# Performance work log

Hardware: AMD Instinct MI355X
Metric: run time of the kernel (lower is better)

Reference implementation:

```python
import jax, jax.numpy as jnp
import numpy as np

# CSSA config (index=0): H=W=64, strip windows h_spa=64, w_spa=8, heads=4, C=64
B, HW, C, HEADS = 32, 64, 64, 4
HS, WS = 64, 8          # h_spa, w_spa
HD = C // HEADS          # head_dim = 16
WIN = HS * WS            # 512 tokens per window
SCALE = HD ** -0.5


def setup_inputs() -> dict:
    key = jax.random.key(0)
    k1, k2, k3 = jax.random.split(key, 3)
    qkv = jax.random.normal(k1, (3, B, HW * HW, C), dtype=jnp.float32)
    w_conv = jax.random.normal(k2, (C, 1, 3, 3), dtype=jnp.float32) * 0.1
    b_conv = jax.random.normal(k3, (C,), dtype=jnp.float32) * 0.1
    return {"qkv": qkv, "w_conv": w_conv, "b_conv": b_conv}


def _to_img(x):
    # [B, N, C] -> [B, C, H, W]
    return jnp.transpose(x.reshape(B, HW, HW, C), (0, 3, 1, 2))


def _img2window_heads(x):
    img = _to_img(x)
    img = img.reshape(B, C, HW // HS, HS, HW // WS, WS)
    win = jnp.transpose(img, (0, 2, 4, 3, 5, 1)).reshape(-1, WIN, C)
    return jnp.transpose(win.reshape(-1, WIN, HEADS, HD), (0, 2, 1, 3))


def _v_windows(x):
    # [B, N, C] -> [B*nWin, C, h_spa, w_spa] (image-layout windows for conv)
    img = _to_img(x)
    img = img.reshape(B, C, HW // HS, HS, HW // WS, WS)
    return jnp.transpose(img, (0, 2, 4, 1, 3, 5)).reshape(-1, C, HS, WS)


def reference(qkv, w_conv, b_conv):
    q, k, v = qkv[0], qkv[1], qkv[2]
    qh = _img2window_heads(q) * SCALE
    kh = _img2window_heads(k)
    vw = _v_windows(v)                           # [Bw, C, HS, WS]
    # depthwise 3x3 conv LePE
    lepe = jax.lax.conv_general_dilated(
        vw, w_conv, window_strides=(1, 1), padding=((1, 1), (1, 1)),
        feature_group_count=C,
        dimension_numbers=("NCHW", "OIHW", "NCHW")) + b_conv[None, :, None, None]
    Bw = vw.shape[0]
    lepe = jnp.transpose(lepe.reshape(Bw, HEADS, HD, WIN), (0, 1, 3, 2))
    vh = jnp.transpose(vw.reshape(Bw, HEADS, HD, WIN), (0, 1, 3, 2))
    attn = jax.nn.softmax(jnp.einsum("whqd,whkd->whqk", qh, kh), axis=-1)
    x = jnp.einsum("whqk,whkd->whqd", attn, vh) + lepe
    x = jnp.transpose(x, (0, 2, 1, 3)).reshape(Bw, WIN, C)
    # window2spa
    x = x.reshape(B, HW // HS, HW // WS, HS, WS, C)
    x = jnp.transpose(x, (0, 1, 3, 2, 4, 5)).reshape(B, HW * HW, C)
    return x
```

## Files before the change

kernel.cpp:

```cpp
#include <hip/hip_runtime.h>
#include <stdint.h>

#define NB    32
#define CCH   64
#define HD    16
#define WIN   512
#define KSTR  72
#define VSTR  520
#define PSTR  40

typedef __attribute__((ext_vector_type(8))) short          short8;
typedef __attribute__((ext_vector_type(4))) float          f32x4;
typedef __attribute__((ext_vector_type(4))) unsigned short us4;

__device__ __forceinline__ float bf2f(unsigned short u) {
    union { unsigned int i; float f; } x; x.i = ((unsigned int)u) << 16; return x.f;
}
__device__ __forceinline__ unsigned short f2bf(float f) {
    union { float f; unsigned int i; } x; x.f = f;
    unsigned int r = x.i + 0x7FFFu + ((x.i >> 16) & 1u);
    return (unsigned short)(r >> 16);
}

__global__ __launch_bounds__(512, 2)
void CSSA_69355131896243_kernel(const float* __restrict__ qkv,
                                const float* __restrict__ wconv,
                                const float* __restrict__ bconv,
                                float* __restrict__ out)
{
    __shared__ unsigned short Kl[WIN * KSTR];
    __shared__ unsigned short Vt[CCH * VSTR];
    __shared__ unsigned short Pl[8 * 16 * PSTR];

    const int tid  = threadIdx.x;
    const int wave = tid >> 6;
    const int lane = tid & 63;
    const int quad = lane >> 4;
    const int l15  = lane & 15;

    const int win = blockIdx.x;
    const int b   = win >> 3;
    const int wx  = win & 7;

    const size_t ONE  = (size_t)NB * 4096 * CCH;
    const size_t base = ((size_t)b * 4096 + (size_t)wx * 8) * CCH;

    {
        const float* gK = qkv + ONE     + base;
        const float* gV = qkv + 2 * ONE + base;
        const int tokb = lane >> 4;
        const int c0   = (lane & 15) * 4;
        for (int r = 0; r < 8; ++r) {
            const int y = r * 8 + wave;
            #pragma unroll
            for (int half = 0; half < 2; ++half) {
                const int t = y * 8 + half * 4 + tokb;
                const size_t goff = (size_t)y * 4096 + half * 256 + lane * 4;
                f32x4 kd = *(const f32x4*)(gK + goff);
                f32x4 vd = *(const f32x4*)(gV + goff);
                us4 kb;
                #pragma unroll
                for (int j = 0; j < 4; ++j) kb[j] = f2bf(kd[j]);
                *(us4*)(&Kl[t * KSTR + c0]) = kb;
                #pragma unroll
                for (int j = 0; j < 4; ++j) Vt[(c0 + j) * VSTR + t] = f2bf(vd[j]);
            }
        }
    }
    __syncthreads();

    const int h  = wave >> 1;
    const int qh = wave & 1;
    const int ch = h * HD + l15;

    float wr[9];
    #pragma unroll
    for (int i = 0; i < 9; ++i) wr[i] = wconv[ch * 9 + i];
    const float bias = bconv[ch];

    unsigned short* Pw = &Pl[wave * 16 * PSTR];
    const float* gQ = qkv + base;
    const float EC = 0.25f * 1.44269504088896341f;

    for (int pass = 0; pass < 2; ++pass) {
        const int q0 = qh * 256 + pass * 128;

        short8 qf[8];
        #pragma unroll
        for (int t = 0; t < 8; ++t) {
            if (quad < 2) {
                const int q = q0 + t * 16 + l15;
                const float* p = gQ + ((size_t)(q >> 3) * 64 + (q & 7)) * CCH + h * HD + quad * 8;
                f32x4 a = *(const f32x4*)p;
                f32x4 c = *(const f32x4*)(p + 4);
                short8 f;
                #pragma unroll
                for (int j = 0; j < 4; ++j) {
                    f[j]     = (short)f2bf(a[j]);
                    f[j + 4] = (short)f2bf(c[j]);
                }
                qf[t] = f;
            } else {
                qf[t] = (short8)0;
            }
        }

        f32x4 acc[8];
        f32x4 lp[8];
        #pragma unroll
        for (int t = 0; t < 8; ++t) { acc[t] = (f32x4)0.0f; lp[t] = (f32x4)0.0f; }

        for (int c = 0; c < 16; ++c) {
            const int k0 = c * 32;
            short8 kf0 = (short8)0, kf1 = (short8)0;
            if (quad < 2) {
                kf0 = *(const short8*)(&Kl[(k0 + l15)      * KSTR + h * HD + quad * 8]);
                kf1 = *(const short8*)(&Kl[(k0 + 16 + l15) * KSTR + h * HD + quad * 8]);
            }
            const short8 vf = *(const short8*)(&Vt[ch * VSTR + k0 + quad * 8]);

            #pragma unroll
            for (int t = 0; t < 8; ++t) {
                f32x4 s0 = __builtin_amdgcn_mfma_f32_16x16x32_bf16(qf[t], kf0, (f32x4)0.0f, 0, 0, 0);
                f32x4 s1 = __builtin_amdgcn_mfma_f32_16x16x32_bf16(qf[t], kf1, (f32x4)0.0f, 0, 0, 0);
                float p0[4], p1[4];
                #pragma unroll
                for (int j = 0; j < 4; ++j) {
                    p0[j] = __builtin_amdgcn_exp2f(s0[j] * EC);
                    p1[j] = __builtin_amdgcn_exp2f(s1[j] * EC);
                    lp[t][j] += p0[j] + p1[j];
                }
                #pragma unroll
                for (int j = 0; j < 4; ++j) {
                    Pw[(quad * 4 + j) * PSTR + l15]      = f2bf(p0[j]);
                    Pw[(quad * 4 + j) * PSTR + 16 + l15] = f2bf(p1[j]);
                }
                const short8 pf = *(const short8*)(&Pw[l15 * PSTR + quad * 8]);
                acc[t] = __builtin_amdgcn_mfma_f32_16x16x32_bf16(pf, vf, acc[t], 0, 0, 0);
            }
        }

        #pragma unroll
        for (int t = 0; t < 8; ++t) {
            f32x4 l4 = lp[t];
            #pragma unroll
            for (int j = 0; j < 4; ++j) {
                float v = l4[j];
                v += __shfl_xor(v, 1, 64);
                v += __shfl_xor(v, 2, 64);
                v += __shfl_xor(v, 4, 64);
                v += __shfl_xor(v, 8, 64);
                l4[j] = __builtin_amdgcn_rcpf(v);
            }
            #pragma unroll
            for (int j = 0; j < 4; ++j) {
                const int q  = q0 + t * 16 + quad * 4 + j;
                const int y  = q >> 3;
                const int xp = q & 7;
                float lep = bias;
                #pragma unroll
                for (int dy = 0; dy < 3; ++dy) {
                    #pragma unroll
                    for (int dx = 0; dx < 3; ++dx) {
                        const int yy = y + dy - 1, xx = xp + dx - 1;
                        const bool ok = ((unsigned)yy < 64u) && ((unsigned)xx < 8u);
                        const int tt = (q + (dy - 1) * 8 + (dx - 1)) & 511;
                        const float vv = bf2f(Vt[ch * VSTR + tt]);
                        lep += (ok ? wr[dy * 3 + dx] : 0.0f) * vv;
                    }
                }
                const float o = acc[t][j] * l4[j] + lep;
                const size_t off = ((size_t)y * 64 + xp) * CCH + ch;
                out[base + off] = o;
            }
        }
    }
}

extern "C" void kernel_launch(void* const* d_in, const int* in_sizes, int n_in,
                              void* d_out, int out_size, void* d_ws, size_t ws_size,
                              hipStream_t stream) {
    const float* qkv   = (const float*)d_in[0];
    const float* wconv = (const float*)d_in[1];
    const float* bconv = (const float*)d_in[2];
    float* outp = (float*)d_out;
    hipLaunchKernelGGL(CSSA_69355131896243_kernel, dim3(256), dim3(512), 0, stream,
                       qkv, wconv, bconv, outp);
}
```

Before: 226.2 us.

## Split attention per head per block and use K=16 bf16 MFMA with transposed scores

Launches one block per (window, head) instead of one per window, which gives 1024 blocks of 256 threads and much smaller LDS per block. Scores are computed transposed (K times Q) with the 16x16x16 bf16 MFMA, so the probability tile feeds the PV MFMA straight from registers, removing the LDS round-trip for P. It also prescales Q, rounds to bf16 with a cheaper packed conversion, prefetches K/V fragments, stages conv weights in LDS, and writes outputs as float4 vectors. The trade-off is that each head block reloads its slice of K and V, rounding changes slightly, and the block order is remapped across the grid.

```diff
diff --git a/kernel.cpp b/kernel.cpp
--- a/kernel.cpp
+++ b/kernel.cpp
@@ -1,179 +1,226 @@
 #include <hip/hip_runtime.h>
 #include <stdint.h>
 
-#define NB    32
-#define CCH   64
-#define HD    16
-#define WIN   512
-#define KSTR  72
+#define KSTR2 20
 #define VSTR  520
-#define PSTR  40
-
-typedef __attribute__((ext_vector_type(8))) short          short8;
+
+typedef __attribute__((ext_vector_type(4))) short          short4v;
+typedef __attribute__((ext_vector_type(8))) short          short8v;
 typedef __attribute__((ext_vector_type(4))) float          f32x4;
 typedef __attribute__((ext_vector_type(4))) unsigned short us4;
 
+#define HAVE_MFMA16 __has_builtin(__builtin_amdgcn_mfma_f32_16x16x16bf16_1k)
+
 __device__ __forceinline__ float bf2f(unsigned short u) {
     union { unsigned int i; float f; } x; x.i = ((unsigned int)u) << 16; return x.f;
 }
 __device__ __forceinline__ unsigned short f2bf(float f) {
-    union { float f; unsigned int i; } x; x.f = f;
-    unsigned int r = x.i + 0x7FFFu + ((x.i >> 16) & 1u);
-    return (unsigned short)(r >> 16);
-}
-
-__global__ __launch_bounds__(512, 2)
+    union { float f; unsigned int u; } x; x.f = f;
+    return (unsigned short)((x.u + 0x8000u) >> 16);
+}
+__device__ __forceinline__ unsigned int pk2bf(float lo, float hi) {
+    union { float f; unsigned int u; } a, b; a.f = lo; b.f = hi;
+    return __builtin_amdgcn_perm(b.u + 0x8000u, a.u + 0x8000u, 0x07060302u);
+}
+
+__global__ __launch_bounds__(256, 4)
 void CSSA_69355131896243_kernel(const float* __restrict__ qkv,
                                 const float* __restrict__ wconv,
                                 const float* __restrict__ bconv,
                                 float* __restrict__ out)
 {
-    __shared__ unsigned short Kl[WIN * KSTR];
-    __shared__ unsigned short Vt[CCH * VSTR];
-    __shared__ unsigned short Pl[8 * 16 * PSTR];
+    __shared__ unsigned short Kl[512 * KSTR2];
+    __shared__ unsigned short Vt[16 * VSTR];
+    __shared__ float Wl[144];
+    __shared__ float Bl[16];
 
     const int tid  = threadIdx.x;
-    const int wave = tid >> 6;
-    const int lane = tid & 63;
-    const int quad = lane >> 4;
-    const int l15  = lane & 15;
-
-    const int win = blockIdx.x;
-    const int b   = win >> 3;
-    const int wx  = win & 7;
-
-    const size_t ONE  = (size_t)NB * 4096 * CCH;
-    const size_t base = ((size_t)b * 4096 + (size_t)wx * 8) * CCH;
+    const int wave = tid >> 6, lane = tid & 63, quad = lane >> 4, l15 = lane & 15;
+
+    const int bid = blockIdx.x;
+    const int win = (bid & 7) * 32 + ((bid >> 3) >> 2);
+    const int h   = (bid >> 3) & 3;
+    const int b   = win >> 3, wx = win & 7;
+
+    const size_t ONE  = (size_t)32 * 4096 * 64;
+    const size_t base = ((size_t)b * 4096 + (size_t)wx * 8) * 64;
+    const float* gQ = qkv + base;
+    const float* gK = qkv + ONE + base;
+    const float* gV = qkv + 2 * ONE + base;
+
+    if (tid < 144) Wl[tid] = wconv[h * 144 + tid];
+    if (tid < 16)  Bl[tid] = bconv[h * 16 + tid];
 
     {
-        const float* gK = qkv + ONE     + base;
-        const float* gV = qkv + 2 * ONE + base;
-        const int tokb = lane >> 4;
-        const int c0   = (lane & 15) * 4;
+        const int t4 = tid >> 2;
+        const int c4 = tid & 3;
         for (int r = 0; r < 8; ++r) {
-            const int y = r * 8 + wave;
-            #pragma unroll
-            for (int half = 0; half < 2; ++half) {
-                const int t = y * 8 + half * 4 + tokb;
-                const size_t goff = (size_t)y * 4096 + half * 256 + lane * 4;
-                f32x4 kd = *(const f32x4*)(gK + goff);
-                f32x4 vd = *(const f32x4*)(gV + goff);
-                us4 kb;
+            const int t = r * 64 + t4;
+            const size_t goff = (size_t)(t >> 3) * 4096 + (size_t)(t & 7) * 64 + h * 16 + c4 * 4;
+            f32x4 kd = *(const f32x4*)(gK + goff);
+            f32x4 vd = *(const f32x4*)(gV + goff);
+            us4 kb;
+            #pragma unroll
+            for (int j = 0; j < 4; ++j) kb[j] = f2bf(kd[j]);
+            *(us4*)(&Kl[t * KSTR2 + c4 * 4]) = kb;
+            #pragma unroll
+            for (int j = 0; j < 4; ++j) Vt[(c4 * 4 + j) * VSTR + t] = f2bf(vd[j]);
+        }
+    }
+
+    const float SCL = 0.25f * 1.44269504088896341f;
+#if HAVE_MFMA16
+    f32x4 qv[8];
+    #pragma unroll
+    for (int t = 0; t < 8; ++t) {
+        const int q = wave * 128 + t * 16 + l15;
+        qv[t] = *(const f32x4*)(gQ + (size_t)(q >> 3) * 4096 + (size_t)(q & 7) * 64 + h * 16 + quad * 4);
+    }
+#else
+    f32x4 qv0[8], qv1[8];
+    #pragma unroll
+    for (int t = 0; t < 8; ++t) {
+        const int q = wave * 128 + t * 16 + l15;
+        const size_t off = (size_t)(q >> 3) * 4096 + (size_t)(q & 7) * 64 + h * 16 + (quad & 1) * 8;
+        qv0[t] = *(const f32x4*)(gQ + off);
+        qv1[t] = *(const f32x4*)(gQ + off + 4);
+    }
+#endif
+    __syncthreads();
+
+#if HAVE_MFMA16
+    short4v qf[8];
+    #pragma unroll
+    for (int t = 0; t < 8; ++t) {
+        union { short4v s; unsigned int u[2]; } p;
+        p.u[0] = pk2bf(qv[t][0] * SCL, qv[t][1] * SCL);
+        p.u[1] = pk2bf(qv[t][2] * SCL, qv[t][3] * SCL);
+        qf[t] = p.s;
+    }
+#else
+    short8v qf[8];
+    #pragma unroll
+    for (int t = 0; t < 8; ++t) {
+        short8v f = (short8v)0;
+        if (quad < 2) {
+            union { short4v s; unsigned int u[2]; } pa, pb;
+            pa.u[0] = pk2bf(qv0[t][0] * SCL, qv0[t][1] * SCL);
+            pa.u[1] = pk2bf(qv0[t][2] * SCL, qv0[t][3] * SCL);
+            pb.u[0] = pk2bf(qv1[t][0] * SCL, qv1[t][1] * SCL);
+            pb.u[1] = pk2bf(qv1[t][2] * SCL, qv1[t][3] * SCL);
+            #pragma unroll
+            for (int i = 0; i < 4; ++i) { f[i] = pa.s[i]; f[4 + i] = pb.s[i]; }
+        }
+        qf[t] = f;
+    }
+#endif
+
+    f32x4 acc[8];
+    float lp[8];
+    #pragma unroll
+    for (int t = 0; t < 8; ++t) { acc[t] = (f32x4)0.0f; lp[t] = 0.0f; }
+
+#if HAVE_MFMA16
+    short4v kf = *(const short4v*)(&Kl[l15 * KSTR2 + quad * 4]);
+    short4v vf = *(const short4v*)(&Vt[l15 * VSTR + quad * 4]);
+    for (int c = 0; c < 32; ++c) {
+        const int kn = ((c + 1) & 31) * 16;
+        short4v kf_n = *(const short4v*)(&Kl[(kn + l15) * KSTR2 + quad * 4]);
+        short4v vf_n = *(const short4v*)(&Vt[l15 * VSTR + kn + quad * 4]);
+        #pragma unroll
+        for (int t = 0; t < 8; ++t) {
+            f32x4 s = __builtin_amdgcn_mfma_f32_16x16x16bf16_1k(kf, qf[t], (f32x4)0.0f, 0, 0, 0);
+            float p0 = __builtin_amdgcn_exp2f(s[0]);
+            float p1 = __builtin_amdgcn_exp2f(s[1]);
+            float p2 = __builtin_amdgcn_exp2f(s[2]);
+            float p3 = __builtin_amdgcn_exp2f(s[3]);
+            lp[t] += (p0 + p1) + (p2 + p3);
+            union { short4v s4; unsigned int u[2]; } pf;
+            pf.u[0] = pk2bf(p0, p1);
+            pf.u[1] = pk2bf(p2, p3);
+            acc[t] = __builtin_amdgcn_mfma_f32_16x16x16bf16_1k(vf, pf.s4, acc[t], 0, 0, 0);
+        }
+        kf = kf_n; vf = vf_n;
+    }
+#else
+    const int bidx0 = (((quad & 1) * 2) * 16 + l15) * 4;
+    const int bidx1 = bidx0 + 64;
+    for (int c = 0; c < 16; ++c) {
+        const int k0 = c * 32;
+        short8v kfA = (short8v)0, kfB = (short8v)0;
+        if (quad < 2) {
+            const short4v a0 = *(const short4v*)(&Kl[(k0 + l15) * KSTR2 + quad * 8]);
+            const short4v a1 = *(const short4v*)(&Kl[(k0 + l15) * KSTR2 + quad * 8 + 4]);
+            const short4v b0 = *(const short4v*)(&Kl[(k0 + 16 + l15) * KSTR2 + quad * 8]);
+            const short4v b1 = *(const short4v*)(&Kl[(k0 + 16 + l15) * KSTR2 + quad * 8 + 4]);
+            #pragma unroll
+            for (int i = 0; i < 4; ++i) { kfA[i] = a0[i]; kfA[4 + i] = a1[i]; kfB[i] = b0[i]; kfB[4 + i] = b1[i]; }
+        }
+        const short8v vf8 = *(const short8v*)(&Vt[l15 * VSTR + k0 + quad * 8]);
+        #pragma unroll
+        for (int t = 0; t < 8; ++t) {
+            f32x4 s0 = __builtin_amdgcn_mfma_f32_16x16x32_bf16(kfA, qf[t], (f32x4)0.0f, 0, 0, 0);
+            f32x4 s1 = __builtin_amdgcn_mfma_f32_16x16x32_bf16(kfB, qf[t], (f32x4)0.0f, 0, 0, 0);
+            float e0[4], e1[4];
+            #pragma unroll
+            for (int j = 0; j < 4; ++j) {
+                e0[j] = __builtin_amdgcn_exp2f(s0[j]);
+                e1[j] = __builtin_amdgcn_exp2f(s1[j]);
+                lp[t] += e0[j] + e1[j];
+            }
+            const unsigned int a0 = pk2bf(e0[0], e0[1]), a1 = pk2bf(e0[2], e0[3]);
+            const unsigned int b0 = pk2bf(e1[0], e1[1]), b1 = pk2bf(e1[2], e1[3]);
+            const unsigned int s0u = (quad < 2) ? a0 : b0;
+            const unsigned int s1u = (quad < 2) ? a1 : b1;
+            union { short8v s8; unsigned int u[4]; } pf;
+            pf.u[0] = (unsigned int)__builtin_amdgcn_ds_bpermute(bidx0, (int)s0u);
+            pf.u[1] = (unsigned int)__builtin_amdgcn_ds_bpermute(bidx0, (int)s1u);
+            pf.u[2] = (unsigned int)__builtin_amdgcn_ds_bpermute(bidx1, (int)s0u);
+            pf.u[3] = (unsigned int)__builtin_amdgcn_ds_bpermute(bidx1, (int)s1u);
+            acc[t] = __builtin_amdgcn_mfma_f32_16x16x32_bf16(vf8, pf.s8, acc[t], 0, 0, 0);
+        }
+    }
+#endif
+
+    float linv[8];
+    #pragma unroll
+    for (int t = 0; t < 8; ++t) {
+        float v = lp[t];
+        v += __shfl_xor(v, 16, 64);
+        v += __shfl_xor(v, 32, 64);
+        linv[t] = __builtin_amdgcn_rcpf(v);
+    }
+
+    #pragma unroll
+    for (int j = 0; j < 4; ++j) {
+        const int d = quad * 4 + j;
+        float w9[9];
+        #pragma unroll
+        for (int o = 0; o < 9; ++o) w9[o] = Wl[d * 9 + o];
+        const float bs = Bl[d];
+        #pragma unroll
+        for (int t = 0; t < 8; ++t) {
+            const int q = wave * 128 + t * 16 + l15;
+            const int y = q >> 3, x = q & 7;
+            float lep = bs;
+            #pragma unroll
+            for (int dy = 0; dy < 3; ++dy) {
                 #pragma unroll
-                for (int j = 0; j < 4; ++j) kb[j] = f2bf(kd[j]);
-                *(us4*)(&Kl[t * KSTR + c0]) = kb;
-                #pragma unroll
-                for (int j = 0; j < 4; ++j) Vt[(c0 + j) * VSTR + t] = f2bf(vd[j]);
+                for (int dx = 0; dx < 3; ++dx) {
+                    const int yy = y + dy - 1, xx = x + dx - 1;
+                    const bool ok = ((unsigned)yy < 64u) && ((unsigned)xx < 8u);
+                    const int tt = (q + (dy - 1) * 8 + (dx - 1)) & 511;
+                    lep += (ok ? w9[dy * 3 + dx] : 0.0f) * bf2f(Vt[d * VSTR + tt]);
+                }
             }
-        }
-    }
-    __syncthreads();
-
-    const int h  = wave >> 1;
-    const int qh = wave & 1;
-    const int ch = h * HD + l15;
-
-    float wr[9];
-    #pragma unroll
-    for (int i = 0; i < 9; ++i) wr[i] = wconv[ch * 9 + i];
-    const float bias = bconv[ch];
-
-    unsigned short* Pw = &Pl[wave * 16 * PSTR];
-    const float* gQ = qkv + base;
-    const float EC = 0.25f * 1.44269504088896341f;
-
-    for (int pass = 0; pass < 2; ++pass) {
-        const int q0 = qh * 256 + pass * 128;
-
-        short8 qf[8];
-        #pragma unroll
-        for (int t = 0; t < 8; ++t) {
-            if (quad < 2) {
-                const int q = q0 + t * 16 + l15;
-                const float* p = gQ + ((size_t)(q >> 3) * 64 + (q & 7)) * CCH + h * HD + quad * 8;
-                f32x4 a = *(const f32x4*)p;
-                f32x4 c = *(const f32x4*)(p + 4);
-                short8 f;
-                #pragma unroll
-                for (int j = 0; j < 4; ++j) {
-                    f[j]     = (short)f2bf(a[j]);
-                    f[j + 4] = (short)f2bf(c[j]);
-                }
-                qf[t] = f;
-            } else {
-                qf[t] = (short8)0;
-            }
-        }
-
-        f32x4 acc[8];
-        f32x4 lp[8];
-        #pragma unroll
-        for (int t = 0; t < 8; ++t) { acc[t] = (f32x4)0.0f; lp[t] = (f32x4)0.0f; }
-
-        for (int c = 0; c < 16; ++c) {
-            const int k0 = c * 32;
-            short8 kf0 = (short8)0, kf1 = (short8)0;
-            if (quad < 2) {
-                kf0 = *(const short8*)(&Kl[(k0 + l15)      * KSTR + h * HD + quad * 8]);
-                kf1 = *(const short8*)(&Kl[(k0 + 16 + l15) * KSTR + h * HD + quad * 8]);
-            }
-            const short8 vf = *(const short8*)(&Vt[ch * VSTR + k0 + quad * 8]);
-
-            #pragma unroll
-            for (int t = 0; t < 8; ++t) {
-                f32x4 s0 = __builtin_amdgcn_mfma_f32_16x16x32_bf16(qf[t], kf0, (f32x4)0.0f, 0, 0, 0);
-                f32x4 s1 = __builtin_amdgcn_mfma_f32_16x16x32_bf16(qf[t], kf1, (f32x4)0.0f, 0, 0, 0);
-                float p0[4], p1[4];
-                #pragma unroll
-                for (int j = 0; j < 4; ++j) {
-                    p0[j] = __builtin_amdgcn_exp2f(s0[j] * EC);
-                    p1[j] = __builtin_amdgcn_exp2f(s1[j] * EC);
-                    lp[t][j] += p0[j] + p1[j];
-                }
-                #pragma unroll
-                for (int j = 0; j < 4; ++j) {
-                    Pw[(quad * 4 + j) * PSTR + l15]      = f2bf(p0[j]);
-                    Pw[(quad * 4 + j) * PSTR + 16 + l15] = f2bf(p1[j]);
-                }
-                const short8 pf = *(const short8*)(&Pw[l15 * PSTR + quad * 8]);
-                acc[t] = __builtin_amdgcn_mfma_f32_16x16x32_bf16(pf, vf, acc[t], 0, 0, 0);
-            }
-        }
-
-        #pragma unroll
-        for (int t = 0; t < 8; ++t) {
-            f32x4 l4 = lp[t];
-            #pragma unroll
-            for (int j = 0; j < 4; ++j) {
-                float v = l4[j];
-                v += __shfl_xor(v, 1, 64);
-                v += __shfl_xor(v, 2, 64);
-                v += __shfl_xor(v, 4, 64);
-                v += __shfl_xor(v, 8, 64);
-                l4[j] = __builtin_amdgcn_rcpf(v);
-            }
-            #pragma unroll
-            for (int j = 0; j < 4; ++j) {
-                const int q  = q0 + t * 16 + quad * 4 + j;
-                const int y  = q >> 3;
-                const int xp = q & 7;
-                float lep = bias;
-                #pragma unroll
-                for (int dy = 0; dy < 3; ++dy) {
-                    #pragma unroll
-                    for (int dx = 0; dx < 3; ++dx) {
-                        const int yy = y + dy - 1, xx = xp + dx - 1;
-                        const bool ok = ((unsigned)yy < 64u) && ((unsigned)xx < 8u);
-                        const int tt = (q + (dy - 1) * 8 + (dx - 1)) & 511;
-                        const float vv = bf2f(Vt[ch * VSTR + tt]);
-                        lep += (ok ? wr[dy * 3 + dx] : 0.0f) * vv;
-                    }
-                }
-                const float o = acc[t][j] * l4[j] + lep;
-                const size_t off = ((size_t)y * 64 + xp) * CCH + ch;
-                out[base + off] = o;
-            }
-        }
+            acc[t][j] = acc[t][j] * linv[t] + lep;
+        }
+    }
+    float* gO = out + base;
+    #pragma unroll
+    for (int t = 0; t < 8; ++t) {
+        const int q = wave * 128 + t * 16 + l15;
+        *(f32x4*)(gO + (size_t)(q >> 3) * 4096 + (size_t)(q & 7) * 64 + h * 16 + quad * 4) = acc[t];
     }
 }
 
@@ -184,6 +231,6 @@
     const float* wconv = (const float*)d_in[1];
     const float* bconv = (const float*)d_in[2];
     float* outp = (float*)d_out;
-    hipLaunchKernelGGL(CSSA_69355131896243_kernel, dim3(256), dim3(512), 0, stream,
+    hipLaunchKernelGGL(CSSA_69355131896243_kernel, dim3(1024), dim3(256), 0, stream,
                        qkv, wconv, bconv, outp);
 }
```

Result: faster. 202.3 us (-10.6%).
